# Kernel optimization log

Measured on AMD Instinct MI355X. Metric: run time of the kernel, lower is better.

## Reference

```python
import jax, jax.numpy as jnp
import numpy as np

DIM_V = 512
NUM_HEADS = 8
LN_EPS = 1e-5


def _layernorm(x):
    # LayerNorm over last dim, no affine (simplified_layer_norm=True)
    mu = jnp.mean(x, axis=-1, keepdims=True)
    var = jnp.mean(jnp.square(x - mu), axis=-1, keepdims=True)
    return (x - mu) * jax.lax.rsqrt(var + LN_EPS)


def setup_inputs() -> dict:
    key = jax.random.key(0)
    ks = jax.random.split(key, 12)
    B, Nq, Nk, dQ, dK, dV = 16, 1024, 1024, 512, 512, DIM_V
    s = 0.02
    return {
        "Q": jax.random.normal(ks[0], (B, Nq, dQ), jnp.float32),
        "K": jax.random.normal(ks[1], (B, Nk, dK), jnp.float32),
        "Wq": jax.random.normal(ks[2], (dQ, dV), jnp.float32) * s,
        "bq": jnp.zeros((dV,), jnp.float32),
        "Wk": jax.random.normal(ks[3], (dK, dV), jnp.float32) * s,
        "bk": jnp.zeros((dV,), jnp.float32),
        "Wv": jax.random.normal(ks[4], (dK, dV), jnp.float32) * s,
        "bv": jnp.zeros((dV,), jnp.float32),
        "Wo": jax.random.normal(ks[5], (dV, dV), jnp.float32) * s,
        "bo": jnp.zeros((dV,), jnp.float32),
    }


def reference(Q, K, Wq, bq, Wk, bk, Wv, bv, Wo, bo):
    H = NUM_HEADS
    dh = DIM_V // H
    q = Q @ Wq + bq            # [B, Nq, dV]
    k = K @ Wk + bk            # [B, Nk, dV]
    v = K @ Wv + bv            # [B, Nk, dV]
    B, Nq, _ = q.shape
    Nk = k.shape[1]
    qh = q.reshape(B, Nq, H, dh)
    kh = k.reshape(B, Nk, H, dh)
    vh = v.reshape(B, Nk, H, dh)
    # NOTE: faithful to source — scale by sqrt(dim_V), not sqrt(head_dim)
    scores = jnp.einsum('bqhd,bkhd->bhqk', qh, kh) / jnp.sqrt(jnp.asarray(DIM_V, q.dtype))
    A = jax.nn.softmax(scores, axis=-1)                    # [B, H, Nq, Nk]
    attn = jnp.einsum('bhqk,bkhd->bqhd', A, vh).reshape(B, Nq, DIM_V)
    O = q + attn               # residual with projected Q
    O = _layernorm(O)          # ln0 (no affine)
    O = O + jax.nn.gelu(O @ Wo + bo, approximate=False)
    O = _layernorm(O)          # ln1 (no affine)
    return O
```

## Files before the change

### kernel.cpp

```cpp
#include <hip/hip_runtime.h>
#include <hip/hip_bf16.h>
#include <math.h>

typedef __bf16 bf16;
typedef __bf16 bf16x8 __attribute__((ext_vector_type(8)));
typedef float  f32x4  __attribute__((ext_vector_type(4)));
typedef float  f32x16 __attribute__((ext_vector_type(16)));
typedef unsigned u32x4 __attribute__((ext_vector_type(4)));

#define MFMA16(a,b,c) __builtin_amdgcn_mfma_f32_16x16x32_bf16((a),(b),(c),0,0,0)
#define MFMA32(a,b,c) __builtin_amdgcn_mfma_f32_32x32x16_bf16((a),(b),(c),0,0,0)
#define KSCALE 0.0637587159f

__device__ __forceinline__ void async16p(const void* g, void* l) {
    __builtin_amdgcn_global_load_lds((const __attribute__((address_space(1))) void*)g,
                                     (__attribute__((address_space(3))) void*)l,
                                     16, 0, 0);
}

__device__ __forceinline__ float fexp2(float x) {
#if __has_builtin(__builtin_amdgcn_exp2f)
    return __builtin_amdgcn_exp2f(x);
#else
    return exp2f(x);
#endif
}

__device__ __forceinline__ unsigned pkbf(float a, float b) {
    union { bf16 h[2]; unsigned u; } x;
    x.h[0] = (bf16)a; x.h[1] = (bf16)b; return x.u;
}

__device__ __forceinline__ void plswap(unsigned &a, unsigned &b) {
#if __has_builtin(__builtin_amdgcn_permlane32_swap)
    auto r = __builtin_amdgcn_permlane32_swap((int)a, (int)b, false, false);
    a = (unsigned)r[0]; b = (unsigned)r[1];
#else
    unsigned sa = (unsigned)__shfl_xor((int)a, 32);
    unsigned sb = (unsigned)__shfl_xor((int)b, 32);
    bool hi = (threadIdx.x & 32) != 0;
    unsigned na = hi ? sb : a;
    unsigned nb = hi ? b  : sa;
    a = na; b = nb;
#endif
}

__global__ __launch_bounds__(256) void prep_w_kernel(
    const float* __restrict__ Wq, const float* __restrict__ Wk,
    const float* __restrict__ Wv, const float* __restrict__ Wo,
    bf16* __restrict__ WqT, bf16* __restrict__ WkT,
    bf16* __restrict__ WvT, bf16* __restrict__ WoT)
{
    __shared__ float tile[32][33];
    const int bx = blockIdx.x;
    const float* W; bf16* T;
    switch (bx >> 8) {
      case 0: W=Wq; T=WqT; break;
      case 1: W=Wk; T=WkT; break;
      case 2: W=Wv; T=WvT; break;
      default: W=Wo; T=WoT; break;
    }
    const int rest = bx & 255;
    const int k0 = (rest & 15) * 32, n0 = (rest >> 4) * 32;
    const int tx = threadIdx.x & 31, ty = threadIdx.x >> 5;
    #pragma unroll
    for (int i=0;i<32;i+=8)
        tile[ty+i][tx] = W[(size_t)(k0+ty+i)*512 + n0+tx];
    __syncthreads();
    #pragma unroll
    for (int i=0;i<32;i+=8)
        T[(size_t)(n0+ty+i)*512 + k0+tx] = (bf16)tile[tx][ty+i];
}

__global__ __launch_bounds__(256, 2) void gemm_proj_kernel(
    const float* __restrict__ Qf, const float* __restrict__ Kf,
    const bf16* __restrict__ WqT, const bf16* __restrict__ WkT,
    const bf16* __restrict__ WvT,
    const float* __restrict__ bq, const float* __restrict__ bk,
    const float* __restrict__ bv,
    bf16* __restrict__ qbb, bf16* __restrict__ kbb, bf16* __restrict__ vT)
{
    __shared__ __align__(16) char smem[65536];
    float* As32 = (float*)smem;
    bf16*  Bs   = (bf16*)(smem + 32768);
    bf16*  Lt   = (bf16*)smem;

    const int x = blockIdx.x;
    const bool isQ = (x < 256);
    int m0, n0;
    const float* A; const bf16 *BT0, *BT1; const float *bb0, *bb1;
    if (isQ) {
        m0 = (x >> 1) * 128; n0 = (x & 1) * 128;
        A = Qf; BT0 = WqT + (size_t)n0*512; BT1 = WqT + (size_t)(n0+256)*512;
        bb0 = bq + n0; bb1 = bq + n0 + 256;
    } else {
        int r = x - 256;
        m0 = (r >> 2) * 128; n0 = (r & 3) * 128;
        A = Kf; BT0 = WkT + (size_t)n0*512; BT1 = WvT + (size_t)n0*512;
        bb0 = bk + n0; bb1 = bv + n0;
    }

    const int tid = threadIdx.x;
    const int lane = tid & 63, wave = tid >> 6;
    const int qd = lane >> 4, lr = lane & 15;
    const int wm = (wave & 1) * 64, wn = (wave >> 1) * 64;

    const float* gA = A + (size_t)(m0 + (tid>>3))*512 + (((tid&7)^((tid>>3)&7))*4);
    const int bgr = ((tid & 3) ^ ((tid >> 3) & 3)) * 8;
    const bf16* gB0 = BT0 + (size_t)(tid>>2)*512 + bgr;
    const bf16* gB1 = BT1 + (size_t)(tid>>2)*512 + bgr;

    f32x4 acc[2][4][4];
    #pragma unroll
    for (int p=0;p<2;p++)
      #pragma unroll
      for (int i=0;i<4;i++)
        #pragma unroll
        for (int j=0;j<4;j++) acc[p][i][j] = (f32x4){0,0,0,0};

    auto stage = [&](int buf, int k0) {
        float* lA = As32 + buf*4096 + wave*256;
        #pragma unroll
        for (int i=0;i<4;i++)
            async16p(gA + k0 + (size_t)i*32*512, lA + i*1024);
        bf16* lB0 = Bs + buf*8192 + wave*512;
        async16p(gB0 + k0,                  lB0);
        async16p(gB0 + k0 + (size_t)64*512, lB0 + 2048);
        bf16* lB1 = Bs + buf*8192 + 4096 + wave*512;
        async16p(gB1 + k0,                  lB1);
        async16p(gB1 + k0 + (size_t)64*512, lB1 + 2048);
    };

    stage(0, 0);
    for (int t = 0; t < 16; ++t) {
        const int cur = t & 1;
        __builtin_amdgcn_sched_barrier(0);
        __builtin_amdgcn_s_barrier();
        if (t < 15) {
            stage(cur ^ 1, (t+1)*32);
            asm volatile("s_waitcnt vmcnt(8)" ::: "memory");
        } else {
            asm volatile("s_waitcnt vmcnt(0)" ::: "memory");
        }
        __builtin_amdgcn_s_barrier();

        const float* Ab = As32 + cur*4096;
        const bf16*  Bb = Bs   + cur*8192;
        bf16x8 af[4], bfr[2][4];
        #pragma unroll
        for (int mi=0;mi<4;mi++) {
            int row = wm + mi*16 + lr;
            f32x4 f0 = *(f32x4*)(Ab + row*32 + (((qd*2  )^(lr&7))*4));
            f32x4 f1 = *(f32x4*)(Ab + row*32 + (((qd*2+1)^(lr&7))*4));
            bf16x8 a;
            a[0]=(bf16)f0[0]; a[1]=(bf16)f0[1]; a[2]=(bf16)f0[2]; a[3]=(bf16)f0[3];
            a[4]=(bf16)f1[0]; a[5]=(bf16)f1[1]; a[6]=(bf16)f1[2]; a[7]=(bf16)f1[3];
            af[mi] = a;
        }
        #pragma unroll
        for (int p=0;p<2;p++)
          #pragma unroll
          for (int ni=0;ni<4;ni++)
            bfr[p][ni] = *(bf16x8*)(Bb + p*4096 + (wn+ni*16+lr)*32
                                       + ((qd^((lr>>1)&3))*8));
        #pragma unroll
        for (int p=0;p<2;p++)
          #pragma unroll
          for (int mi=0;mi<4;mi++)
            #pragma unroll
            for (int ni=0;ni<4;ni++)
              acc[p][mi][ni] = MFMA16(af[mi], bfr[p][ni], acc[p][mi][ni]);
    }

    if (isQ) {
        #pragma unroll
        for (int p=0;p<2;p++) {
            const float* bb = p ? bb1 : bb0;
            #pragma unroll
            for (int ni=0;ni<4;ni++) {
                int nl = wn + ni*16 + lr;
                int n = n0 + p*256 + nl;
                float bv0 = bb[nl];
                #pragma unroll
                for (int mi=0;mi<4;mi++) {
                    int mb = m0 + wm + mi*16 + qd*4;
                    #pragma unroll
                    for (int r=0;r<4;r++)
                        qbb[(size_t)(mb+r)*512 + n] = (bf16)(acc[p][mi][ni][r] + bv0);
                }
            }
        }
    } else {
        #pragma unroll
        for (int ni=0;ni<4;ni++) {
            int nl = wn + ni*16 + lr;
            int n = n0 + nl;
            float bv0 = bb0[nl];
            #pragma unroll
            for (int mi=0;mi<4;mi++) {
                int mb = m0 + wm + mi*16 + qd*4;
                #pragma unroll
                for (int r=0;r<4;r++)
                    kbb[(size_t)(mb+r)*512 + n] = (bf16)((acc[0][mi][ni][r] + bv0)*KSCALE);
            }
        }
        const int b = m0 >> 10, tok0 = m0 & 1023;
        const int row = tid >> 2, ch = tid & 3;
        #pragma unroll
        for (int half = 0; half < 2; ++half) {
            __syncthreads();
            if ((wn >> 6) == half) {
                #pragma unroll
                for (int ni=0;ni<4;ni++) {
                    int nl = ni*16 + lr;
                    float bvv = bb1[half*64 + nl];
                    #pragma unroll
                    for (int mi=0;mi<4;mi++)
                      #pragma unroll
                      for (int r=0;r<4;r++) {
                        int col = wm + mi*16 + qd*4 + r;
                        Lt[nl*128 + ((((col>>3)^(nl&7))<<3) | (col&7))]
                            = (bf16)(acc[1][mi][ni][r] + bvv);
                      }
                }
            }
            __syncthreads();
            const int h = (n0 >> 6) + half;
            bf16* dst = vT + ((size_t)((b*8 + h)*64 + row))*1024 + tok0 + ch*32;
            #pragma unroll
            for (int s=0;s<4;s++) {
                int g = (ch*4 + s) ^ (row & 7);
                *(uint4*)(dst + s*8) = *(uint4*)(Lt + row*128 + g*8);
            }
        }
    }
}

__global__ __launch_bounds__(256, 4) void attn_kernel(
    const bf16* __restrict__ qb, const bf16* __restrict__ kb,
    const bf16* __restrict__ vT, bf16* __restrict__ attnb)
{
    const int x = blockIdx.x;
    const int qt = x >> 7, h = x & 7, b = (x & 127) >> 3;
    const int tid = threadIdx.x, lane = tid & 63, wave = tid >> 6;
    const int l = lane & 31, hi = lane >> 5;
    const int q0w = qt*128 + wave*32;

    __shared__ __align__(16) bf16 kv[2][2][4096];
    __shared__ float ls[4][32];

    bf16x8 aq[4];
    {
        const bf16* qrow = qb + ((size_t)(b*1024 + q0w + l))*512 + h*64 + hi*8;
        #pragma unroll
        for (int st=0; st<4; ++st) aq[st] = *(const bf16x8*)(qrow + st*16);
    }

    const int srow = lane >> 3;
    const int sgA  = (lane & 7) ^ srow ^ wave;
    const int sgB  = sgA ^ 4;
    const bf16* kg0 = kb + ((size_t)(b*1024 + wave*8 + srow))*512      + h*64 + sgA*8;
    const bf16* kg1 = kb + ((size_t)(b*1024 + wave*8 + srow + 32))*512 + h*64 + sgB*8;
    const bf16* vg0 = vT + ((size_t)((b*8 + h)*64 + wave*8 + srow))*1024      + sgA*8;
    const bf16* vg1 = vT + ((size_t)((b*8 + h)*64 + wave*8 + srow + 32))*1024 + sgB*8;

    auto stage = [&](int buf, int t) {
        const size_t ko = (size_t)t*64*512;
        async16p(kg0 + ko,     &kv[buf][0][wave*512]);
        async16p(kg1 + ko,     &kv[buf][0][2048 + wave*512]);
        async16p(vg0 + t*64,   &kv[buf][1][wave*512]);
        async16p(vg1 + t*64,   &kv[buf][1][2048 + wave*512]);
    };

    f32x16 accO[2];
    accO[0] = (f32x16)0.f; accO[1] = (f32x16)0.f;
    float lsum = 0.f;
    const int kx = (l & 7) ^ (l >> 3);

    stage(0, 0);
    for (int t=0; t<16; ++t) {
        const int cur = t & 1;
        __builtin_amdgcn_sched_barrier(0);
        __builtin_amdgcn_s_barrier();
        if (t < 15) {
            stage(cur ^ 1, t + 1);
            asm volatile("s_waitcnt vmcnt(4)" ::: "memory");
        } else {
            asm volatile("s_waitcnt vmcnt(0)" ::: "memory");
        }
        __builtin_amdgcn_s_barrier();

        const bf16* Ks = kv[cur][0];
        const bf16* Vs = kv[cur][1];

        u32x4 paf[4];
        #pragma unroll
        for (int kb2=0; kb2<2; ++kb2) {
            f32x16 sT = (f32x16)0.f;
            __builtin_amdgcn_s_setprio(1);
            #pragma unroll
            for (int st=0; st<4; ++st) {
                bf16x8 kf = *(const bf16x8*)(Ks + (kb2*32 + l)*64
                               + (((st*2 + hi) ^ kx ^ (kb2<<2))*8));
                sT = MFMA32(kf, aq[st], sT);
            }
            __builtin_amdgcn_s_setprio(0);
            unsigned u[8];
            #pragma unroll
            for (int m=0; m<8; ++m) {
                float e0 = fexp2(sT[2*m]);
                float e1 = fexp2(sT[2*m+1]);
                lsum += e0 + e1;
                u[m] = pkbf(e0, e1);
            }
            #pragma unroll
            for (int sb=0; sb<2; ++sb) {
                unsigned a0=u[4*sb], a1=u[4*sb+1], a2=u[4*sb+2], a3=u[4*sb+3];
                plswap(a0, a2);
                plswap(a1, a3);
                paf[kb2*2 + sb] = (u32x4){a0, a1, a2, a3};
            }
        }
        __builtin_amdgcn_s_setprio(1);
        #pragma unroll
        for (int db=0; db<2; ++db) {
            f32x16 a = accO[db];
            #pragma unroll
            for (int st=0; st<4; ++st) {
                bf16x8 vf = *(const bf16x8*)(Vs + (db*32 + l)*64
                               + (((st*2 + hi) ^ kx ^ (db<<2))*8));
                u32x4 pp = paf[st];
                bf16x8 pf = *(bf16x8*)&pp;
                a = MFMA32(pf, vf, a);
            }
            accO[db] = a;
        }
        __builtin_amdgcn_s_setprio(0);
    }

    lsum += __shfl_xor(lsum, 32);
    ls[wave][l] = lsum;
    __syncthreads();

    #pragma unroll
    for (int g=0; g<4; ++g) {
        f32x4 lv = *(const f32x4*)(&ls[wave][g*8 + hi*4]);
        f32x4 inv;
        #pragma unroll
        for (int i=0;i<4;i++) inv[i] = 1.f / lv[i];
        #pragma unroll
        for (int db=0; db<2; ++db) {
            #pragma unroll
            for (int i=0;i<4;i++) {
                int r = g*4 + i;
                int qrow = q0w + g*8 + hi*4 + i;
                size_t idx = ((size_t)(b*1024 + qrow))*512 + h*64 + db*32 + l;
                float o = accO[db][r] * inv[i] + (float)qb[idx];
                attnb[idx] = (bf16)o;
            }
        }
    }
}

__global__ __launch_bounds__(256) void ln0_kernel(
    const bf16* __restrict__ attnb, bf16* __restrict__ Obf)
{
    const int wave = threadIdx.x >> 6, lane = threadIdx.x & 63;
    const int row = blockIdx.x*4 + wave;
    const size_t base = (size_t)row*512 + lane*8;
    bf16x8 av = *(const bf16x8*)(attnb + base);
    float x[8];
    #pragma unroll
    for (int i=0;i<8;i++) x[i] = (float)av[i];
    float s1 = 0.f, s2 = 0.f;
    #pragma unroll
    for (int i=0;i<8;i++){ s1 += x[i]; s2 += x[i]*x[i]; }
    #pragma unroll
    for (int off=1; off<64; off<<=1) { s1 += __shfl_xor(s1, off); s2 += __shfl_xor(s2, off); }
    float mu  = s1 * (1.f/512.f);
    float var = s2 * (1.f/512.f) - mu*mu;
    float rstd = rsqrtf(var + 1e-5f);
    bf16x8 ob;
    #pragma unroll
    for (int i=0;i<8;i++) ob[i] = (bf16)((x[i]-mu)*rstd);
    *(bf16x8*)(Obf + base) = ob;
}

__global__ __launch_bounds__(256, 4) void gemm_o_kernel(
    const bf16* __restrict__ Obf, const bf16* __restrict__ WoT,
    const float* __restrict__ bo, bf16* __restrict__ xb)
{
    __shared__ __align__(16) char smem[24576];
    bf16* As = (bf16*)smem;
    bf16* Bs = (bf16*)(smem + 8192);
    const int m0 = blockIdx.x * 64, n0 = blockIdx.y * 128;
    const int tid = threadIdx.x;
    const int lane = tid & 63, wave = tid >> 6;
    const int qd = lane >> 4, lr = lane & 15;
    const int wm = (wave & 1) * 32, wn = (wave >> 1) * 64;

    const int bgr = ((tid & 3) ^ ((tid >> 3) & 3)) * 8;
    const bf16* gA = Obf + (size_t)(m0 + (tid>>2))*512 + bgr;
    const bf16* gB = WoT + (size_t)(n0 + (tid>>2))*512 + bgr;

    f32x4 acc[2][4];
    #pragma unroll
    for (int i=0;i<2;i++)
      #pragma unroll
      for (int j=0;j<4;j++) acc[i][j] = (f32x4){0,0,0,0};

    auto stage = [&](int buf, int k0) {
        async16p(gA + k0,                  As + buf*2048 + wave*512);
        bf16* lB = Bs + buf*4096 + wave*512;
        async16p(gB + k0,                  lB);
        async16p(gB + k0 + (size_t)64*512, lB + 2048);
    };

    stage(0, 0);
    for (int t = 0; t < 16; ++t) {
        const int cur = t & 1;
        __builtin_amdgcn_sched_barrier(0);
        __builtin_amdgcn_s_barrier();
        if (t < 15) {
            stage(cur ^ 1, (t+1)*32);
            asm volatile("s_waitcnt vmcnt(3)" ::: "memory");
        } else {
            asm volatile("s_waitcnt vmcnt(0)" ::: "memory");
        }
        __builtin_amdgcn_s_barrier();

        const bf16* Ab = As + cur*2048;
        const bf16* Bb = Bs + cur*4096;
        bf16x8 af[2], bfr[4];
        #pragma unroll
        for (int mi=0;mi<2;mi++)
            af[mi] = *(bf16x8*)(Ab + (wm+mi*16+lr)*32 + ((qd^((lr>>1)&3))*8));
        #pragma unroll
        for (int ni=0;ni<4;ni++)
            bfr[ni] = *(bf16x8*)(Bb + (wn+ni*16+lr)*32 + ((qd^((lr>>1)&3))*8));
        #pragma unroll
        for (int mi=0;mi<2;mi++)
          #pragma unroll
          for (int ni=0;ni<4;ni++)
            acc[mi][ni] = MFMA16(af[mi], bfr[ni], acc[mi][ni]);
    }

    #pragma unroll
    for (int ni=0;ni<4;ni++) {
        int n = n0 + wn + ni*16 + lr;
        float bv = bo[n];
        #pragma unroll
        for (int mi=0;mi<2;mi++) {
            int mb = m0 + wm + mi*16 + qd*4;
            #pragma unroll
            for (int r=0;r<4;r++) {
                float g = acc[mi][ni][r] + bv;
                float gelu = 0.5f * g * (1.f + erff(g * 0.70710678118654752f));
                size_t idx = (size_t)(mb+r)*512 + n;
                xb[idx] = (bf16)((float)Obf[idx] + gelu);
            }
        }
    }
}

__global__ __launch_bounds__(256) void ln1_kernel(
    const bf16* __restrict__ xb, float* __restrict__ out)
{
    const int wave = threadIdx.x >> 6, lane = threadIdx.x & 63;
    const int row = blockIdx.x*4 + wave;
    const size_t base = (size_t)row*512 + lane*8;
    bf16x8 xv = *(const bf16x8*)(xb + base);
    float x[8];
    #pragma unroll
    for (int i=0;i<8;i++) x[i] = (float)xv[i];
    float s1 = 0.f, s2 = 0.f;
    #pragma unroll
    for (int i=0;i<8;i++){ s1 += x[i]; s2 += x[i]*x[i]; }
    #pragma unroll
    for (int off=1; off<64; off<<=1) { s1 += __shfl_xor(s1, off); s2 += __shfl_xor(s2, off); }
    float mu  = s1 * (1.f/512.f);
    float var = s2 * (1.f/512.f) - mu*mu;
    float rstd = rsqrtf(var + 1e-5f);
    float4 o0 = {(x[0]-mu)*rstd,(x[1]-mu)*rstd,(x[2]-mu)*rstd,(x[3]-mu)*rstd};
    float4 o1 = {(x[4]-mu)*rstd,(x[5]-mu)*rstd,(x[6]-mu)*rstd,(x[7]-mu)*rstd};
    *(float4*)(out + base)     = o0;
    *(float4*)(out + base + 4) = o1;
}

extern "C" void kernel_launch(void* const* d_in, const int* in_sizes, int n_in,
                              void* d_out, int out_size, void* d_ws, size_t ws_size,
                              hipStream_t stream)
{
    (void)in_sizes; (void)n_in; (void)out_size; (void)ws_size;
    const float* Q  = (const float*)d_in[0];
    const float* K  = (const float*)d_in[1];
    const float* Wq = (const float*)d_in[2];
    const float* bq = (const float*)d_in[3];
    const float* Wk = (const float*)d_in[4];
    const float* bk = (const float*)d_in[5];
    const float* Wv = (const float*)d_in[6];
    const float* bv = (const float*)d_in[7];
    const float* Wo = (const float*)d_in[8];
    const float* bo = (const float*)d_in[9];
    float* out = (float*)d_out;

    const size_t nTok = (size_t)16*1024*512;
    char* p = (char*)d_ws;
    auto alloc = [&](size_t bytes)->char* {
        char* r = p; p += (bytes + 255) & ~(size_t)255; return r;
    };
    bf16* WqT   = (bf16*)alloc(512*512*2);
    bf16* WkT   = (bf16*)alloc(512*512*2);
    bf16* WvT   = (bf16*)alloc(512*512*2);
    bf16* WoT   = (bf16*)alloc(512*512*2);
    bf16* qbb   = (bf16*)alloc(nTok*2);
    bf16* kbb   = (bf16*)alloc(nTok*2);
    bf16* vT    = (bf16*)alloc(nTok*2);
    bf16* attnb = (bf16*)alloc(nTok*2);
    bf16* Obf   = (bf16*)alloc(nTok*2);
    bf16* xb    = (bf16*)alloc(nTok*2);

    prep_w_kernel<<<1024, 256, 0, stream>>>(Wq, Wk, Wv, Wo, WqT, WkT, WvT, WoT);
    gemm_proj_kernel<<<768, 256, 0, stream>>>(Q, K, WqT, WkT, WvT,
                                              bq, bk, bv, qbb, kbb, vT);
    attn_kernel<<<dim3(1024), 256, 0, stream>>>(qbb, kbb, vT, attnb);
    ln0_kernel<<<4096, 256, 0, stream>>>(attnb, Obf);
    gemm_o_kernel<<<dim3(256,4), 256, 0, stream>>>(Obf, WoT, bo, xb);
    ln1_kernel<<<4096, 256, 0, stream>>>(xb, out);
}
```

Baseline: 251.5 us.

## Load fp32 A operand directly into registers, drop LDS staging and remap tiles

The projection GEMM no longer stages the fp32 A tile through LDS. Each wave now loads its own A fragments from global memory into registers, prefetching one k-step ahead, and the vmcnt waits are adjusted to match. This halves the shared-memory footprint, which may allow more blocks per CU, and removes LDS write/read traffic for A. The block-to-tile mapping is also changed so consecutive blocks walk along M with the same N slice, improving weight reuse in cache. The cost is more registers, and the A loads from global are strided row reads, so each wave refetches rows that other waves also need.

```diff
diff --git a/kernel.cpp b/kernel.cpp
--- a/kernel.cpp
+++ b/kernel.cpp
@@ -80,22 +80,21 @@
     const float* __restrict__ bv,
     bf16* __restrict__ qbb, bf16* __restrict__ kbb, bf16* __restrict__ vT)
 {
-    __shared__ __align__(16) char smem[65536];
-    float* As32 = (float*)smem;
-    bf16*  Bs   = (bf16*)(smem + 32768);
-    bf16*  Lt   = (bf16*)smem;
+    __shared__ __align__(16) char smem[32768];
+    bf16* Bs = (bf16*)smem;
+    bf16* Lt = (bf16*)smem;
 
     const int x = blockIdx.x;
     const bool isQ = (x < 256);
     int m0, n0;
     const float* A; const bf16 *BT0, *BT1; const float *bb0, *bb1;
     if (isQ) {
-        m0 = (x >> 1) * 128; n0 = (x & 1) * 128;
+        m0 = (x & 127) * 128; n0 = (x >> 7) * 128;
         A = Qf; BT0 = WqT + (size_t)n0*512; BT1 = WqT + (size_t)(n0+256)*512;
         bb0 = bq + n0; bb1 = bq + n0 + 256;
     } else {
         int r = x - 256;
-        m0 = (r >> 2) * 128; n0 = (r & 3) * 128;
+        m0 = (r & 127) * 128; n0 = (r >> 7) * 128;
         A = Kf; BT0 = WkT + (size_t)n0*512; BT1 = WvT + (size_t)n0*512;
         bb0 = bk + n0; bb1 = bv + n0;
     }
@@ -105,11 +104,12 @@
     const int qd = lane >> 4, lr = lane & 15;
     const int wm = (wave & 1) * 64, wn = (wave >> 1) * 64;
 
-    const float* gA = A + (size_t)(m0 + (tid>>3))*512 + (((tid&7)^((tid>>3)&7))*4);
     const int bgr = ((tid & 3) ^ ((tid >> 3) & 3)) * 8;
     const bf16* gB0 = BT0 + (size_t)(tid>>2)*512 + bgr;
     const bf16* gB1 = BT1 + (size_t)(tid>>2)*512 + bgr;
 
+    const float* aRow = A + (size_t)(m0 + wm + lr)*512 + qd*8;
+
     f32x4 acc[2][4][4];
     #pragma unroll
     for (int p=0;p<2;p++)
@@ -119,10 +119,6 @@
         for (int j=0;j<4;j++) acc[p][i][j] = (f32x4){0,0,0,0};
 
     auto stage = [&](int buf, int k0) {
-        float* lA = As32 + buf*4096 + wave*256;
-        #pragma unroll
-        for (int i=0;i<4;i++)
-            async16p(gA + k0 + (size_t)i*32*512, lA + i*1024);
         bf16* lB0 = Bs + buf*8192 + wave*512;
         async16p(gB0 + k0,                  lB0);
         async16p(gB0 + k0 + (size_t)64*512, lB0 + 2048);
@@ -131,32 +127,44 @@
         async16p(gB1 + k0 + (size_t)64*512, lB1 + 2048);
     };
 
+    f32x4 aP[8];
+    auto loadA = [&](int k0) {
+        #pragma unroll
+        for (int mi=0;mi<4;mi++) {
+            const float* p = aRow + (size_t)mi*16*512 + k0;
+            aP[2*mi]   = *(const f32x4*)p;
+            aP[2*mi+1] = *(const f32x4*)(p + 4);
+        }
+    };
+
     stage(0, 0);
+    loadA(0);
     for (int t = 0; t < 16; ++t) {
         const int cur = t & 1;
         __builtin_amdgcn_sched_barrier(0);
         __builtin_amdgcn_s_barrier();
         if (t < 15) {
             stage(cur ^ 1, (t+1)*32);
+            asm volatile("s_waitcnt vmcnt(12)" ::: "memory");
+        } else {
             asm volatile("s_waitcnt vmcnt(8)" ::: "memory");
-        } else {
-            asm volatile("s_waitcnt vmcnt(0)" ::: "memory");
-        }
+        }
+        __builtin_amdgcn_sched_barrier(0);
         __builtin_amdgcn_s_barrier();
 
-        const float* Ab = As32 + cur*4096;
-        const bf16*  Bb = Bs   + cur*8192;
-        bf16x8 af[4], bfr[2][4];
+        bf16x8 af[4];
         #pragma unroll
         for (int mi=0;mi<4;mi++) {
-            int row = wm + mi*16 + lr;
-            f32x4 f0 = *(f32x4*)(Ab + row*32 + (((qd*2  )^(lr&7))*4));
-            f32x4 f1 = *(f32x4*)(Ab + row*32 + (((qd*2+1)^(lr&7))*4));
+            f32x4 f0 = aP[2*mi], f1 = aP[2*mi+1];
             bf16x8 a;
             a[0]=(bf16)f0[0]; a[1]=(bf16)f0[1]; a[2]=(bf16)f0[2]; a[3]=(bf16)f0[3];
             a[4]=(bf16)f1[0]; a[5]=(bf16)f1[1]; a[6]=(bf16)f1[2]; a[7]=(bf16)f1[3];
             af[mi] = a;
         }
+        if (t < 15) loadA((t+1)*32);
+
+        const bf16* Bb = Bs + cur*8192;
+        bf16x8 bfr[2][4];
         #pragma unroll
         for (int p=0;p<2;p++)
           #pragma unroll
```

After: 282.4 us. +12.3%, slower.

## Fold LayerNorm0 into output GEMM epilogue via Wo column sums

Applied to the files above, without the earlier changes.

Replaces the materialized normalized LN0 output with a stats-only pass (mean, rstd per row), and runs the Wo GEMM directly on the un-normalized residual. The epilogue applies normalization algebraically via rstd*acc - rstd*mu*colsum(Wo), where the column sums come from a small new kernel over fp32 Wo. This removes one full bf16 tensor write and its re-read, at the cost of an extra tiny kernel and a numerics change: the GEMM now sees bf16 un-normalized values, and the normalization is applied after accumulation using fp32 column sums rather than the bf16 weights actually multiplied.

```diff
diff --git a/kernel.cpp b/kernel.cpp
--- a/kernel.cpp
+++ b/kernel.cpp
@@ -70,6 +70,16 @@
     #pragma unroll
     for (int i=0;i<32;i+=8)
         T[(size_t)(n0+ty+i)*512 + k0+tx] = (bf16)tile[tx][ty+i];
+}
+
+__global__ __launch_bounds__(256) void csum_kernel(
+    const float* __restrict__ Wo, float* __restrict__ csum)
+{
+    const int n = blockIdx.x*256 + threadIdx.x;
+    float s = 0.f;
+    #pragma unroll 8
+    for (int k=0;k<512;k++) s += Wo[(size_t)k*512 + n];
+    csum[n] = s;
 }
 
 __global__ __launch_bounds__(256, 2) void gemm_proj_kernel(
@@ -362,8 +372,8 @@
     }
 }
 
-__global__ __launch_bounds__(256) void ln0_kernel(
-    const bf16* __restrict__ attnb, bf16* __restrict__ Obf)
+__global__ __launch_bounds__(256) void ln_stats_kernel(
+    const bf16* __restrict__ attnb, float2* __restrict__ stats)
 {
     const int wave = threadIdx.x >> 6, lane = threadIdx.x & 63;
     const int row = blockIdx.x*4 + wave;
@@ -380,15 +390,13 @@
     float mu  = s1 * (1.f/512.f);
     float var = s2 * (1.f/512.f) - mu*mu;
     float rstd = rsqrtf(var + 1e-5f);
-    bf16x8 ob;
-    #pragma unroll
-    for (int i=0;i<8;i++) ob[i] = (bf16)((x[i]-mu)*rstd);
-    *(bf16x8*)(Obf + base) = ob;
+    if (lane == 0) stats[row] = make_float2(mu, rstd);
 }
 
 __global__ __launch_bounds__(256, 4) void gemm_o_kernel(
-    const bf16* __restrict__ Obf, const bf16* __restrict__ WoT,
-    const float* __restrict__ bo, bf16* __restrict__ xb)
+    const bf16* __restrict__ attnb, const bf16* __restrict__ WoT,
+    const float* __restrict__ bo, const float* __restrict__ csum,
+    const float2* __restrict__ stats, bf16* __restrict__ xb)
 {
     __shared__ __align__(16) char smem[24576];
     bf16* As = (bf16*)smem;
@@ -400,8 +408,8 @@
     const int wm = (wave & 1) * 32, wn = (wave >> 1) * 64;
 
     const int bgr = ((tid & 3) ^ ((tid >> 3) & 3)) * 8;
-    const bf16* gA = Obf + (size_t)(m0 + (tid>>2))*512 + bgr;
-    const bf16* gB = WoT + (size_t)(n0 + (tid>>2))*512 + bgr;
+    const bf16* gA = attnb + (size_t)(m0 + (tid>>2))*512 + bgr;
+    const bf16* gB = WoT   + (size_t)(n0 + (tid>>2))*512 + bgr;
 
     f32x4 acc[2][4];
     #pragma unroll
@@ -445,19 +453,28 @@
             acc[mi][ni] = MFMA16(af[mi], bfr[ni], acc[mi][ni]);
     }
 
+    float csn[4], bon[4];
     #pragma unroll
     for (int ni=0;ni<4;ni++) {
         int n = n0 + wn + ni*16 + lr;
-        float bv = bo[n];
-        #pragma unroll
-        for (int mi=0;mi<2;mi++) {
-            int mb = m0 + wm + mi*16 + qd*4;
-            #pragma unroll
-            for (int r=0;r<4;r++) {
-                float g = acc[mi][ni][r] + bv;
+        csn[ni] = csum[n];
+        bon[ni] = bo[n];
+    }
+    #pragma unroll
+    for (int mi=0;mi<2;mi++) {
+        #pragma unroll
+        for (int r=0;r<4;r++) {
+            int row = m0 + wm + mi*16 + qd*4 + r;
+            float2 st = stats[row];
+            float mu = st.x, rstd = st.y;
+            #pragma unroll
+            for (int ni=0;ni<4;ni++) {
+                int n = n0 + wn + ni*16 + lr;
+                float g = rstd*acc[mi][ni][r] - rstd*mu*csn[ni] + bon[ni];
                 float gelu = 0.5f * g * (1.f + erff(g * 0.70710678118654752f));
-                size_t idx = (size_t)(mb+r)*512 + n;
-                xb[idx] = (bf16)((float)Obf[idx] + gelu);
+                size_t idx = (size_t)row*512 + n;
+                float lnx = ((float)attnb[idx] - mu) * rstd;
+                xb[idx] = (bf16)(lnx + gelu);
             }
         }
     }
@@ -509,22 +526,24 @@
     auto alloc = [&](size_t bytes)->char* {
         char* r = p; p += (bytes + 255) & ~(size_t)255; return r;
     };
-    bf16* WqT   = (bf16*)alloc(512*512*2);
-    bf16* WkT   = (bf16*)alloc(512*512*2);
-    bf16* WvT   = (bf16*)alloc(512*512*2);
-    bf16* WoT   = (bf16*)alloc(512*512*2);
-    bf16* qbb   = (bf16*)alloc(nTok*2);
-    bf16* kbb   = (bf16*)alloc(nTok*2);
-    bf16* vT    = (bf16*)alloc(nTok*2);
-    bf16* attnb = (bf16*)alloc(nTok*2);
-    bf16* Obf   = (bf16*)alloc(nTok*2);
-    bf16* xb    = (bf16*)alloc(nTok*2);
+    bf16*   WqT   = (bf16*)alloc(512*512*2);
+    bf16*   WkT   = (bf16*)alloc(512*512*2);
+    bf16*   WvT   = (bf16*)alloc(512*512*2);
+    bf16*   WoT   = (bf16*)alloc(512*512*2);
+    bf16*   qbb   = (bf16*)alloc(nTok*2);
+    bf16*   kbb   = (bf16*)alloc(nTok*2);
+    bf16*   vT    = (bf16*)alloc(nTok*2);
+    bf16*   attnb = (bf16*)alloc(nTok*2);
+    bf16*   xb    = (bf16*)alloc(nTok*2);
+    float*  csum  = (float*)alloc(512*4);
+    float2* stats = (float2*)alloc(16384*8);
 
     prep_w_kernel<<<1024, 256, 0, stream>>>(Wq, Wk, Wv, Wo, WqT, WkT, WvT, WoT);
+    csum_kernel<<<2, 256, 0, stream>>>(Wo, csum);
     gemm_proj_kernel<<<768, 256, 0, stream>>>(Q, K, WqT, WkT, WvT,
                                               bq, bk, bv, qbb, kbb, vT);
     attn_kernel<<<dim3(1024), 256, 0, stream>>>(qbb, kbb, vT, attnb);
-    ln0_kernel<<<4096, 256, 0, stream>>>(attnb, Obf);
-    gemm_o_kernel<<<dim3(256,4), 256, 0, stream>>>(Obf, WoT, bo, xb);
+    ln_stats_kernel<<<4096, 256, 0, stream>>>(attnb, stats);
+    gemm_o_kernel<<<dim3(256,4), 256, 0, stream>>>(attnb, WoT, bo, csum, stats, xb);
     ln1_kernel<<<4096, 256, 0, stream>>>(xb, out);
 }
```

Result: slower. 265.7 us (+5.7%).
